# Optimization experiments

Hardware: AMD Instinct MI355X
Metric: run time of the kernel (lower is better)

The kernel has to match this reference:

```python
import jax, jax.numpy as jnp
import numpy as np

DIM = 384
DIM_HEAD = 384
HEADS = 4
SCALE = (DIM_HEAD / HEADS) ** -0.5  # per-head dim 96


def _chan_layernorm(x, g, eps=1e-5):
    # LayerNorm over channel dim (axis=1), biased variance, scale only
    mean = jnp.mean(x, axis=1, keepdims=True)
    var = jnp.var(x, axis=1, keepdims=True)
    return (x - mean) * jax.lax.rsqrt(var + eps) * g


def setup_inputs() -> dict:
    key = jax.random.key(0)
    k0, k1, k2 = jax.random.split(key, 3)
    x = jax.random.normal(k0, (16, DIM, 64, 64), dtype=jnp.float32)
    prenorm_g = jnp.ones((1, DIM, 1, 1), dtype=jnp.float32)
    Wqkv = jax.random.normal(k1, (3 * DIM_HEAD, DIM), dtype=jnp.float32) * 0.02
    Wout = jax.random.normal(k2, (DIM, DIM_HEAD), dtype=jnp.float32) * 0.02
    bout = jnp.zeros((DIM,), dtype=jnp.float32)
    outnorm_g = jnp.ones((1, DIM, 1, 1), dtype=jnp.float32)
    return {"x": x, "prenorm_g": prenorm_g, "Wqkv": Wqkv,
            "Wout": Wout, "bout": bout, "outnorm_g": outnorm_g}


def reference(x, prenorm_g, Wqkv, Wout, bout, outnorm_g):
    b, c, h, w = x.shape
    n = h * w
    ch = DIM_HEAD // HEADS  # per-head channels

    xn = _chan_layernorm(x, prenorm_g)              # prenorm; residual uses this
    qkv = jnp.einsum('oc,bchw->bohw', Wqkv, xn)     # 1x1 conv, no bias
    q, k, v = jnp.split(qkv, 3, axis=1)             # each [b, dim_head, h, w]

    def to_heads(t):
        return t.reshape(b, HEADS, ch, n)           # b h c (x y)
    q, k, v = to_heads(q), to_heads(k), to_heads(v)

    q = jax.nn.softmax(q, axis=2) * SCALE           # softmax over channel dim
    k = jax.nn.softmax(k, axis=3)                   # softmax over spatial dim

    context = jnp.einsum('bhdn,bhen->bhde', k, v)   # [b,h,ch,ch]
    out = jnp.einsum('bhde,bhdn->bhen', context, q) # [b,h,ch,n]
    out = out.reshape(b, DIM_HEAD, h, w)

    out = jnp.einsum('oc,bchw->bohw', Wout, out) + bout[None, :, None, None]
    out = _chan_layernorm(out, outnorm_g)
    return out + xn
```

## Files before the change

kernel.cpp:

```cpp
#include <hip/hip_runtime.h>
#include <cstdint>
#include <cstddef>


#define P_     65536
#define P96_   6291456
#define ROW_   384
#define NS_    8
#define CHK_   512
#define SCALE_ 0.10206207261596577f
#define EPS_   1e-5f

typedef unsigned short us16;
typedef __attribute__((ext_vector_type(8))) unsigned short ushort8;
typedef __attribute__((ext_vector_type(8))) short short8;
typedef __attribute__((ext_vector_type(4))) float f32x4;
typedef __attribute__((ext_vector_type(2))) unsigned int uint2v;

static __device__ __forceinline__ float bfu2f(us16 u) {
  union { float f; unsigned int i; } x; x.i = ((unsigned int)u) << 16; return x.f;
}
static __device__ __forceinline__ us16 f2bfu(float f) {
  union { float f; unsigned int u; } x; x.f = f;
  unsigned int r = x.u + 0x7fffu + ((x.u >> 16) & 1u);
  return (us16)(r >> 16);
}

#define GLDS16(gp, lp) \
  __builtin_amdgcn_global_load_lds((const __attribute__((address_space(1))) void*)(gp), \
                                   (__attribute__((address_space(3))) void*)(lp), 16, 0, 0)

__global__ __launch_bounds__(256) void k_wcvt(const float* __restrict__ wqkv,
                                              const float* __restrict__ wout,
                                              us16* __restrict__ wbf) {
  int i = (blockIdx.x * 256 + threadIdx.x) * 4;
  const float* s = (i < 442368) ? (wqkv + i) : (wout + (i - 442368));
  wbf[i + 0] = f2bfu(s[0]); wbf[i + 1] = f2bfu(s[1]);
  wbf[i + 2] = f2bfu(s[2]); wbf[i + 3] = f2bfu(s[3]);
}

__global__ __launch_bounds__(256) void k_prenorm(const float* __restrict__ x,
                                                 const float* __restrict__ g,
                                                 us16* __restrict__ xn) {
  __shared__ float gs[384];
  __shared__ float sm[4][64], sq[4][64];
  int t = threadIdx.x;
  for (int c = t; c < 384; c += 256) gs[c] = g[c];
  int qd = t >> 6, pb = t & 63;
  int p = blockIdx.x * 64 + pb;
  int b = p >> 12, pix = p & 4095;
  const float* xb = x + (size_t)b * 1572864 + pix;
  float xv[96];
  float s1 = 0.f, s2 = 0.f;
  #pragma unroll
  for (int i = 0; i < 96; ++i) {
    float v = xb[(size_t)(qd * 96 + i) * 4096];
    xv[i] = v; s1 += v; s2 += v * v;
  }
  sm[qd][pb] = s1; sq[qd][pb] = s2;
  __syncthreads();
  float su = sm[0][pb] + sm[1][pb] + sm[2][pb] + sm[3][pb];
  float ss = sq[0][pb] + sq[1][pb] + sq[2][pb] + sq[3][pb];
  float mean = su * (1.f / 384);
  float var = ss * (1.f / 384) - mean * mean;
  float rs = rsqrtf(var + EPS_);
  us16* ob = xn + (size_t)p * ROW_ + qd * 96;
  #pragma unroll
  for (int c8 = 0; c8 < 12; ++c8) {
    ushort8 u;
    #pragma unroll
    for (int j = 0; j < 8; ++j)
      u[j] = f2bfu((xv[c8 * 8 + j] - mean) * rs * gs[qd * 96 + c8 * 8 + j]);
    *(ushort8*)(ob + c8 * 8) = u;
  }
}

__global__ __launch_bounds__(512, 2) void k_gemm(const us16* __restrict__ src,
                                                 const us16* __restrict__ W,
                                                 us16* __restrict__ dst,
                                                 int MT, int mode) {
  __shared__ __align__(16) us16 As[3 * 16384];
  __shared__ __align__(16) us16 Bs[3 * 8192];
  int i = blockIdx.x;
  int xcd = i & 7, idx = i >> 3;
  int ot = idx % MT;
  int pt = (idx / MT) * 8 + xcd;
  int p0 = pt * 256, o0 = ot * 128;
  int tid = threadIdx.x;
  int wv = tid >> 6, l = tid & 63;
  int wr = wv >> 1, wc = wv & 1;
  int lm = l & 15, kq = l >> 4;
  int lr = l >> 3, lg = l & 7;

  bool rm = (mode != 0) || (ot < 3);
  bool isk = (mode == 0) && (ot >= 3) && (ot < 6);

  const us16* aB[4]; const us16* bB[2];
  int swz = (lg ^ lr) * 8;
  #pragma unroll
  for (int r = 0; r < 4; ++r)
    aB[r] = src + (size_t)(p0 + 64 * r + 8 * wv + lr) * ROW_ + swz;
  #pragma unroll
  for (int r = 0; r < 2; ++r)
    bB[r] = W + (size_t)(o0 + 64 * r + 8 * wv + lr) * ROW_ + swz;

  int aidx[4][2], bidx[4][2];
  #pragma unroll
  for (int ii = 0; ii < 4; ++ii) {
    int row = wr * 64 + ii * 16 + lm;
    #pragma unroll
    for (int ks = 0; ks < 2; ++ks)
      aidx[ii][ks] = row * 8 + ((ks * 4 + kq) ^ (row & 7));
  }
  #pragma unroll
  for (int jj = 0; jj < 4; ++jj) {
    int row = wc * 64 + jj * 16 + lm;
    #pragma unroll
    for (int ks = 0; ks < 2; ++ks)
      bidx[jj][ks] = row * 8 + ((ks * 4 + kq) ^ (row & 7));
  }

  f32x4 acc[4][4];
  #pragma unroll
  for (int a = 0; a < 4; ++a)
    #pragma unroll
    for (int q = 0; q < 4; ++q) acc[a][q] = (f32x4)0.f;

#define STG(t_, b_) do { \
    _Pragma("unroll") \
    for (int r_ = 0; r_ < 4; ++r_) \
      GLDS16(aB[r_] + (t_) * 64, &As[(b_) * 16384 + (64 * r_ + 8 * wv) * 64]); \
    _Pragma("unroll") \
    for (int r_ = 0; r_ < 2; ++r_) \
      GLDS16(bB[r_] + (t_) * 64, &Bs[(b_) * 8192 + (64 * r_ + 8 * wv) * 64]); \
  } while (0)

  STG(0, 0);
  STG(1, 1);
  asm volatile("s_waitcnt vmcnt(6)\n\ts_barrier" ::: "memory");

  #pragma unroll
  for (int t = 0; t < 6; ++t) {
    if (t + 2 < 6) STG(t + 2, (t + 2) % 3);
    const short8* A8 = (const short8*)As + (t % 3) * 2048;
    const short8* B8 = (const short8*)Bs + (t % 3) * 1024;
    __builtin_amdgcn_s_setprio(1);
    #pragma unroll
    for (int ks = 0; ks < 2; ++ks) {
      short8 af[4], bf[4];
      #pragma unroll
      for (int ii = 0; ii < 4; ++ii) af[ii] = A8[aidx[ii][ks]];
      #pragma unroll
      for (int jj = 0; jj < 4; ++jj) bf[jj] = B8[bidx[jj][ks]];
      if (rm) {
        #pragma unroll
        for (int ii = 0; ii < 4; ++ii)
          #pragma unroll
          for (int jj = 0; jj < 4; ++jj)
            acc[ii][jj] = __builtin_amdgcn_mfma_f32_16x16x32_bf16(bf[jj], af[ii], acc[ii][jj], 0, 0, 0);
      } else {
        #pragma unroll
        for (int ii = 0; ii < 4; ++ii)
          #pragma unroll
          for (int jj = 0; jj < 4; ++jj)
            acc[ii][jj] = __builtin_amdgcn_mfma_f32_16x16x32_bf16(af[ii], bf[jj], acc[ii][jj], 0, 0, 0);
      }
    }
    __builtin_amdgcn_s_setprio(0);
    if (t < 5) {
      if (t + 2 < 6)
        asm volatile("s_waitcnt vmcnt(6) lgkmcnt(0)\n\ts_barrier" ::: "memory");
      else
        asm volatile("s_waitcnt vmcnt(0) lgkmcnt(0)\n\ts_barrier" ::: "memory");
    }
  }
#undef STG

  __syncthreads();
  us16* Cs = As;
  const int MS = rm ? 136 : 264;
  #pragma unroll
  for (int ii = 0; ii < 4; ++ii) {
    #pragma unroll
    for (int jj = 0; jj < 4; ++jj) {
      f32x4 v = acc[ii][jj];
      if (isk) {
        #pragma unroll
        for (int r = 0; r < 4; ++r) v[r] = __expf(v[r]);
      }
      alignas(8) us16 b4[4];
      #pragma unroll
      for (int r = 0; r < 4; ++r) b4[r] = f2bfu(v[r]);
      int maj = rm ? (wr * 64 + ii * 16 + lm) : (wc * 64 + jj * 16 + lm);
      int mnr = rm ? (wc * 64 + jj * 16 + kq * 4) : (wr * 64 + ii * 16 + kq * 4);
      *(uint2v*)&Cs[maj * MS + mnr] = *(const uint2v*)b4;
    }
  }
  __syncthreads();

  if (!rm) {
    #pragma unroll
    for (int it = 0; it < 8; ++it) {
      int c = it * 512 + tid;
      int o_l = c >> 5, p8 = c & 31;
      int o = o0 + o_l, sec = o / 96, d = o - sec * 96;
      ushort8 u = *(const ushort8*)&Cs[o_l * 264 + p8 * 8];
      *(ushort8*)(dst + (size_t)sec * P96_ + (size_t)d * P_ + p0 + p8 * 8) = u;
    }
  } else if (mode) {
    #pragma unroll
    for (int it = 0; it < 8; ++it) {
      int c = it * 512 + tid;
      int p_l = c >> 4, ch = c & 15;
      ushort8 u = *(const ushort8*)&Cs[p_l * 136 + ch * 8];
      *(ushort8*)(dst + (size_t)(p0 + p_l) * ROW_ + o0 + ch * 8) = u;
    }
  } else {
    #pragma unroll
    for (int it = 0; it < 8; ++it) {
      int c = it * 512 + tid;
      int p_l = c >> 4, ch = c & 15;
      int o = o0 + ch * 8, sec = o / 96, d = o - sec * 96;
      ushort8 u = *(const ushort8*)&Cs[p_l * 136 + ch * 8];
      *(ushort8*)(dst + (size_t)sec * P96_ + (size_t)(p0 + p_l) * 96 + d) = u;
    }
  }
}

__global__ __launch_bounds__(256) void k_ctx(const us16* __restrict__ qkv,
                                             float* __restrict__ ctxs,
                                             float* __restrict__ zs) {
  __shared__ __align__(16) us16 Ek[96 * 64];
  __shared__ __align__(16) us16 Vv[96 * 64];
  int bh = blockIdx.x, s = blockIdx.y;
  int b = bh >> 2, h = bh & 3;
  const us16* kb = qkv + (size_t)(4 + h) * P96_;
  const us16* vb = qkv + (size_t)(8 + h) * P96_;
  int pbase = b * 4096 + s * CHK_;
  int t = threadIdx.x;
  int wv = t >> 6, l = t & 63;
  int wr = wv >> 1, wc = wv & 1;
  int lm = l & 15, kq = l >> 4;

  f32x4 acc[3][3];
  f32x4 accz[3];
  #pragma unroll
  for (int a = 0; a < 3; ++a) {
    accz[a] = (f32x4)0.f;
    #pragma unroll
    for (int q = 0; q < 3; ++q) acc[a][q] = (f32x4)0.f;
  }
  short8 vone;
  #pragma unroll
  for (int j = 0; j < 8; ++j) vone[j] = (short)0x3F80;

  int srow = wv * 24 + (l >> 3);
  int sgrp = l & 7;

  for (int tile = 0; tile < CHK_ / 64; ++tile) {
    int p0 = pbase + tile * 64;
    #pragma unroll
    for (int c = 0; c < 3; ++c) {
      int r = srow + c * 8;
      int g = sgrp ^ (r & 7);
      GLDS16(kb + (size_t)r * P_ + p0 + g * 8, &Ek[(wv * 24 + c * 8) * 64]);
      GLDS16(vb + (size_t)r * P_ + p0 + g * 8, &Vv[(wv * 24 + c * 8) * 64]);
    }
    __syncthreads();
    const short8* A8 = (const short8*)Ek;
    const short8* B8 = (const short8*)Vv;
    #pragma unroll
    for (int ks = 0; ks < 2; ++ks) {
      short8 af[3], bf[3];
      #pragma unroll
      for (int ii = 0; ii < 3; ++ii) {
        int m = wr * 48 + ii * 16 + lm;
        af[ii] = A8[m * 8 + (((ks * 4 + kq) ^ m) & 7) + ((ks * 4 + kq) & 8)];
        int e = wc * 48 + ii * 16 + lm;
        bf[ii] = B8[e * 8 + (((ks * 4 + kq) ^ e) & 7) + ((ks * 4 + kq) & 8)];
      }
      #pragma unroll
      for (int ii = 0; ii < 3; ++ii)
        #pragma unroll
        for (int jj = 0; jj < 3; ++jj)
          acc[ii][jj] = __builtin_amdgcn_mfma_f32_16x16x32_bf16(af[ii], bf[jj], acc[ii][jj], 0, 0, 0);
      if (wc == 0) {
        #pragma unroll
        for (int ii = 0; ii < 3; ++ii)
          accz[ii] = __builtin_amdgcn_mfma_f32_16x16x32_bf16(af[ii], vone, accz[ii], 0, 0, 0);
      }
    }
    __syncthreads();
  }

  float* cb = ctxs + (size_t)(s * 64 + bh) * 9216;
  #pragma unroll
  for (int ii = 0; ii < 3; ++ii) {
    int m0 = wr * 48 + ii * 16 + kq * 4;
    #pragma unroll
    for (int jj = 0; jj < 3; ++jj) {
      int e = wc * 48 + jj * 16 + lm;
      #pragma unroll
      for (int r = 0; r < 4; ++r)
        cb[(size_t)(m0 + r) * 96 + e] = acc[ii][jj][r];
    }
  }
  if (wc == 0 && lm == 0) {
    #pragma unroll
    for (int ii = 0; ii < 3; ++ii) {
      int m0 = wr * 48 + ii * 16 + kq * 4;
      #pragma unroll
      for (int r = 0; r < 4; ++r)
        zs[(size_t)(s * 64 + bh) * 96 + m0 + r] = accz[ii][r];
    }
  }
}

__global__ __launch_bounds__(256) void k_ctxred(const float* __restrict__ ctxs,
                                                const float* __restrict__ zs,
                                                float* __restrict__ ctx,
                                                float* __restrict__ zr) {
  int bh = blockIdx.x / 9, part = blockIdx.x % 9;
  int t = threadIdx.x;
  int idx = part * 1024 + t * 4;
  f32x4 sum = (f32x4)0.f;
  #pragma unroll
  for (int s = 0; s < NS_; ++s)
    sum += *(const f32x4*)&ctxs[(size_t)(s * 64 + bh) * 9216 + idx];
  *(f32x4*)&ctx[(size_t)bh * 9216 + idx] = sum;
  if (part == 0 && t < 96) {
    float z = 0.f;
    #pragma unroll
    for (int s = 0; s < NS_; ++s) z += zs[(size_t)(s * 64 + bh) * 96 + t];
    zr[bh * 96 + t] = z;
  }
}

__global__ __launch_bounds__(256) void k_attout(const us16* __restrict__ qkv,
                                                const float* __restrict__ ctx,
                                                const float* __restrict__ zr,
                                                us16* __restrict__ attout) {
  __shared__ float cs[9216];
  __shared__ float zrs[96];
  int bh = blockIdx.y, b = bh >> 2, h = bh & 3;
  int t = threadIdx.x;
  const float* cb = ctx + (size_t)bh * 9216;
  for (int i = t; i < 9216; i += 256) cs[i] = cb[i];
  if (t < 96) zrs[t] = 1.0f / zr[bh * 96 + t];
  __syncthreads();
  int p = b * 4096 + blockIdx.x * 256 + t;
  const us16* qrow = qkv + (size_t)h * P96_ + (size_t)p * 96;
  float qv[96];
  #pragma unroll
  for (int c8 = 0; c8 < 12; ++c8) {
    ushort8 u = *(const ushort8*)(qrow + c8 * 8);
    #pragma unroll
    for (int j = 0; j < 8; ++j) qv[c8 * 8 + j] = bfu2f(u[j]);
  }
  float m = -1e30f;
  #pragma unroll
  for (int d = 0; d < 96; ++d) m = fmaxf(m, qv[d]);
  float s = 0.f;
  #pragma unroll
  for (int d = 0; d < 96; ++d) { qv[d] = __expf(qv[d] - m); s += qv[d]; }
  float sc = SCALE_ / s;
  #pragma unroll
  for (int d = 0; d < 96; ++d) qv[d] *= sc * zrs[d];
  us16* ob = attout + (size_t)p * ROW_ + h * 96;
  #pragma unroll 1
  for (int e0 = 0; e0 < 96; e0 += 8) {
    float a0 = 0, a1 = 0, a2 = 0, a3 = 0, a4 = 0, a5 = 0, a6 = 0, a7 = 0;
    #pragma unroll
    for (int d = 0; d < 96; ++d) {
      float qd = qv[d];
      f32x4 c0 = *(const f32x4*)&cs[d * 96 + e0];
      f32x4 c1 = *(const f32x4*)&cs[d * 96 + e0 + 4];
      a0 += qd * c0[0]; a1 += qd * c0[1]; a2 += qd * c0[2]; a3 += qd * c0[3];
      a4 += qd * c1[0]; a5 += qd * c1[1]; a6 += qd * c1[2]; a7 += qd * c1[3];
    }
    ushort8 u;
    u[0] = f2bfu(a0); u[1] = f2bfu(a1); u[2] = f2bfu(a2); u[3] = f2bfu(a3);
    u[4] = f2bfu(a4); u[5] = f2bfu(a5); u[6] = f2bfu(a6); u[7] = f2bfu(a7);
    *(ushort8*)(ob + e0) = u;
  }
}

__global__ __launch_bounds__(256) void k_outnorm(const us16* __restrict__ y,
                                                 const us16* __restrict__ xn,
                                                 const float* __restrict__ bout,
                                                 const float* __restrict__ g,
                                                 float* __restrict__ out) {
  __shared__ float bs[384], gs[384];
  int t = threadIdx.x;
  for (int c = t; c < 384; c += 256) { bs[c] = bout[c]; gs[c] = g[c]; }
  __syncthreads();
  int p = blockIdx.x * 256 + t;
  int b = p >> 12, pix = p & 4095;
  const us16* yb = y + (size_t)p * ROW_;
  const us16* xb = xn + (size_t)p * ROW_;
  float sum = 0.f, sq = 0.f;
  #pragma unroll 4
  for (int c8 = 0; c8 < 48; ++c8) {
    ushort8 u = *(const ushort8*)(yb + c8 * 8);
    #pragma unroll
    for (int j = 0; j < 8; ++j) {
      float v = bfu2f(u[j]) + bs[c8 * 8 + j];
      sum += v; sq += v * v;
    }
  }
  float mean = sum * (1.f / 384);
  float var = sq * (1.f / 384) - mean * mean;
  float rs = rsqrtf(var + EPS_);
  float* oB = out + (size_t)b * 1572864 + pix;
  #pragma unroll 2
  for (int c8 = 0; c8 < 48; ++c8) {
    ushort8 u = *(const ushort8*)(yb + c8 * 8);
    ushort8 ux = *(const ushort8*)(xb + c8 * 8);
    #pragma unroll
    for (int j = 0; j < 8; ++j) {
      int c = c8 * 8 + j;
      float v = bfu2f(u[j]) + bs[c];
      oB[(size_t)c * 4096] = (v - mean) * rs * gs[c] + bfu2f(ux[j]);
    }
  }
}

extern "C" void kernel_launch(void* const* d_in, const int* in_sizes, int n_in,
                              void* d_out, int out_size, void* d_ws, size_t ws_size,
                              hipStream_t stream) {
  const float* x    = (const float*)d_in[0];
  const float* pg   = (const float*)d_in[1];
  const float* wqkv = (const float*)d_in[2];
  const float* wout = (const float*)d_in[3];
  const float* bout = (const float*)d_in[4];
  const float* og   = (const float*)d_in[5];

  char* ws = (char*)d_ws;
  us16*  xn     = (us16*)(ws);
  us16*  qkv    = (us16*)(ws + 50331648);
  us16*  attout = (us16*)(ws + 201326592);
  float* ctxred = (float*)(ws + 251658240);
  float* zred   = (float*)(ws + 254017536);
  us16*  wbf    = (us16*)(ws + 254042112);
  us16*  y      = qkv;
  float* out    = (float*)d_out;
  float* ctxs = (float*)d_out;
  float* zs   = (float*)((char*)d_out + 18874368);

  k_wcvt<<<576, 256, 0, stream>>>(wqkv, wout, wbf);
  k_prenorm<<<1024, 256, 0, stream>>>(x, pg, xn);
  k_gemm<<<2304, 512, 0, stream>>>(xn, wbf, qkv, 9, 0);
  k_ctx<<<dim3(64, NS_), 256, 0, stream>>>(qkv, ctxs, zs);
  k_ctxred<<<576, 256, 0, stream>>>(ctxs, zs, ctxred, zred);
  k_attout<<<dim3(16, 64), 256, 0, stream>>>(qkv, ctxred, zred, attout);
  k_gemm<<<768, 512, 0, stream>>>(attout, wbf + 442368, y, 3, 1);
  k_outnorm<<<256, 256, 0, stream>>>(y, xn, bout, og, out);
}
```

Measured before the change: 476.8 us.

## Fold per-batch context into output projection weights, replacing scalar attout kernel

Instead of computing context^T·q per pixel with scalar FMAs and then applying Wout, the change precomputes a per-batch matrix M = Wout·(context/z)^T with MFMA (context split into bf16 hi/lo parts for precision). The softmaxed, scaled q is written directly, and the final GEMM uses the per-batch M as its weights. This removes the expensive scalar per-pixel 96x96 contraction and the attout intermediate. In exchange it adds a small per-batch weight GEMM and bf16 rounding of the fused matrix.

Result: faster. 434.7 us (-8.8%).

```diff
diff --git a/kernel.cpp b/kernel.cpp
--- a/kernel.cpp
+++ b/kernel.cpp
@@ -94,6 +94,7 @@
 
   bool rm = (mode != 0) || (ot < 3);
   bool isk = (mode == 0) && (ot >= 3) && (ot < 6);
+  const us16* Wb = (mode != 0) ? (W + (size_t)(p0 >> 12) * 147456) : W;
 
   const us16* aB[4]; const us16* bB[2];
   int swz = (lg ^ lr) * 8;
@@ -102,7 +103,7 @@
     aB[r] = src + (size_t)(p0 + 64 * r + 8 * wv + lr) * ROW_ + swz;
   #pragma unroll
   for (int r = 0; r < 2; ++r)
-    bB[r] = W + (size_t)(o0 + 64 * r + 8 * wv + lr) * ROW_ + swz;
+    bB[r] = Wb + (size_t)(o0 + 64 * r + 8 * wv + lr) * ROW_ + swz;
 
   int aidx[4][2], bidx[4][2];
   #pragma unroll
@@ -336,52 +337,115 @@
   }
 }
 
-__global__ __launch_bounds__(256) void k_attout(const us16* __restrict__ qkv,
-                                                const float* __restrict__ ctx,
-                                                const float* __restrict__ zr,
-                                                us16* __restrict__ attout) {
-  __shared__ float cs[9216];
-  __shared__ float zrs[96];
-  int bh = blockIdx.y, b = bh >> 2, h = bh & 3;
+__global__ __launch_bounds__(256) void k_ctxw(const float* __restrict__ ctx,
+                                              const float* __restrict__ zr,
+                                              const us16* __restrict__ wout,
+                                              us16* __restrict__ Mt) {
+  __shared__ __align__(16) us16 Aw[192 * 104];
+  __shared__ __align__(16) us16 Bh[96 * 104];
+  __shared__ __align__(16) us16 Bl[96 * 104];
+  int bh = blockIdx.x >> 1, half = blockIdx.x & 1;
+  int b = bh >> 2, h = bh & 3;
+  int o0 = half * 192;
   int t = threadIdx.x;
+
+  #pragma unroll
+  for (int it = 0; it < 9; ++it) {
+    int c = it * 256 + t;
+    int row = c / 12, e8 = c % 12;
+    ushort8 u = *(const ushort8*)(wout + (size_t)(o0 + row) * 384 + h * 96 + e8 * 8);
+    *(ushort8*)&Aw[row * 104 + e8 * 8] = u;
+  }
   const float* cb = ctx + (size_t)bh * 9216;
-  for (int i = t; i < 9216; i += 256) cs[i] = cb[i];
-  if (t < 96) zrs[t] = 1.0f / zr[bh * 96 + t];
+  #pragma unroll
+  for (int it = 0; it < 9; ++it) {
+    int c = it * 256 + t;
+    int fi = c * 4;
+    int row = fi / 96, e = fi % 96;
+    f32x4 v = *(const f32x4*)&cb[fi];
+    alignas(8) us16 hi[4], lo[4];
+    #pragma unroll
+    for (int r = 0; r < 4; ++r) {
+      hi[r] = f2bfu(v[r]);
+      lo[r] = f2bfu(v[r] - bfu2f(hi[r]));
+    }
+    *(uint2v*)&Bh[row * 104 + e] = *(const uint2v*)hi;
+    *(uint2v*)&Bl[row * 104 + e] = *(const uint2v*)lo;
+  }
   __syncthreads();
-  int p = b * 4096 + blockIdx.x * 256 + t;
-  const us16* qrow = qkv + (size_t)h * P96_ + (size_t)p * 96;
-  float qv[96];
-  #pragma unroll
-  for (int c8 = 0; c8 < 12; ++c8) {
-    ushort8 u = *(const ushort8*)(qrow + c8 * 8);
-    #pragma unroll
-    for (int j = 0; j < 8; ++j) qv[c8 * 8 + j] = bfu2f(u[j]);
-  }
-  float m = -1e30f;
-  #pragma unroll
-  for (int d = 0; d < 96; ++d) m = fmaxf(m, qv[d]);
-  float s = 0.f;
-  #pragma unroll
-  for (int d = 0; d < 96; ++d) { qv[d] = __expf(qv[d] - m); s += qv[d]; }
-  float sc = SCALE_ / s;
-  #pragma unroll
-  for (int d = 0; d < 96; ++d) qv[d] *= sc * zrs[d];
-  us16* ob = attout + (size_t)p * ROW_ + h * 96;
+
+  int wv = t >> 6, l = t & 63;
+  int lm = l & 15, kq = l >> 4;
+  f32x4 acc[3][6];
+  #pragma unroll
+  for (int a = 0; a < 3; ++a)
+    #pragma unroll
+    for (int q = 0; q < 6; ++q) acc[a][q] = (f32x4)0.f;
+
+  const short8* A8 = (const short8*)Aw;
+  const short8* B8h = (const short8*)Bh;
+  const short8* B8l = (const short8*)Bl;
+  #pragma unroll
+  for (int ks = 0; ks < 3; ++ks) {
+    short8 af[3];
+    #pragma unroll
+    for (int ii = 0; ii < 3; ++ii)
+      af[ii] = A8[(wv * 48 + ii * 16 + lm) * 13 + ks * 4 + kq];
+    #pragma unroll
+    for (int jj = 0; jj < 6; ++jj) {
+      short8 bh8 = B8h[(jj * 16 + lm) * 13 + ks * 4 + kq];
+      short8 bl8 = B8l[(jj * 16 + lm) * 13 + ks * 4 + kq];
+      #pragma unroll
+      for (int ii = 0; ii < 3; ++ii) {
+        acc[ii][jj] = __builtin_amdgcn_mfma_f32_16x16x32_bf16(af[ii], bh8, acc[ii][jj], 0, 0, 0);
+        acc[ii][jj] = __builtin_amdgcn_mfma_f32_16x16x32_bf16(af[ii], bl8, acc[ii][jj], 0, 0, 0);
+      }
+    }
+  }
+
+  us16* mb = Mt + (size_t)b * 147456;
+  #pragma unroll
+  for (int jj = 0; jj < 6; ++jj) {
+    int d = jj * 16 + lm;
+    float zinv = 1.0f / zr[bh * 96 + d];
+    #pragma unroll
+    for (int ii = 0; ii < 3; ++ii) {
+      int orow = o0 + wv * 48 + ii * 16 + kq * 4;
+      #pragma unroll
+      for (int r = 0; r < 4; ++r)
+        mb[(size_t)(orow + r) * 384 + h * 96 + d] = f2bfu(acc[ii][jj][r] * zinv);
+    }
+  }
+}
+
+__global__ __launch_bounds__(256) void k_qsm(const us16* __restrict__ qkv,
+                                             us16* __restrict__ Qp) {
+  int p = blockIdx.x * 256 + threadIdx.x;
   #pragma unroll 1
-  for (int e0 = 0; e0 < 96; e0 += 8) {
-    float a0 = 0, a1 = 0, a2 = 0, a3 = 0, a4 = 0, a5 = 0, a6 = 0, a7 = 0;
-    #pragma unroll
-    for (int d = 0; d < 96; ++d) {
-      float qd = qv[d];
-      f32x4 c0 = *(const f32x4*)&cs[d * 96 + e0];
-      f32x4 c1 = *(const f32x4*)&cs[d * 96 + e0 + 4];
-      a0 += qd * c0[0]; a1 += qd * c0[1]; a2 += qd * c0[2]; a3 += qd * c0[3];
-      a4 += qd * c1[0]; a5 += qd * c1[1]; a6 += qd * c1[2]; a7 += qd * c1[3];
-    }
-    ushort8 u;
-    u[0] = f2bfu(a0); u[1] = f2bfu(a1); u[2] = f2bfu(a2); u[3] = f2bfu(a3);
-    u[4] = f2bfu(a4); u[5] = f2bfu(a5); u[6] = f2bfu(a6); u[7] = f2bfu(a7);
-    *(ushort8*)(ob + e0) = u;
+  for (int h = 0; h < 4; ++h) {
+    const us16* qrow = qkv + (size_t)h * P96_ + (size_t)p * 96;
+    float qv[96];
+    #pragma unroll
+    for (int c8 = 0; c8 < 12; ++c8) {
+      ushort8 u = *(const ushort8*)(qrow + c8 * 8);
+      #pragma unroll
+      for (int j = 0; j < 8; ++j) qv[c8 * 8 + j] = bfu2f(u[j]);
+    }
+    float m = -1e30f;
+    #pragma unroll
+    for (int d = 0; d < 96; ++d) m = fmaxf(m, qv[d]);
+    float s = 0.f;
+    #pragma unroll
+    for (int d = 0; d < 96; ++d) { qv[d] = __expf(qv[d] - m); s += qv[d]; }
+    float sc = SCALE_ / s;
+    us16* ob = Qp + (size_t)p * ROW_ + h * 96;
+    #pragma unroll
+    for (int c8 = 0; c8 < 12; ++c8) {
+      ushort8 u;
+      #pragma unroll
+      for (int j = 0; j < 8; ++j) u[j] = f2bfu(qv[c8 * 8 + j] * sc);
+      *(ushort8*)(ob + c8 * 8) = u;
+    }
   }
 }
 
@@ -438,7 +502,7 @@
   char* ws = (char*)d_ws;
   us16*  xn     = (us16*)(ws);
   us16*  qkv    = (us16*)(ws + 50331648);
-  us16*  attout = (us16*)(ws + 201326592);
+  us16*  Qp     = (us16*)(ws + 201326592);
   float* ctxred = (float*)(ws + 251658240);
   float* zred   = (float*)(ws + 254017536);
   us16*  wbf    = (us16*)(ws + 254042112);
@@ -446,13 +510,15 @@
   float* out    = (float*)d_out;
   float* ctxs = (float*)d_out;
   float* zs   = (float*)((char*)d_out + 18874368);
+  us16*  Mt   = (us16*)((char*)d_out + 19070976);
 
   k_wcvt<<<576, 256, 0, stream>>>(wqkv, wout, wbf);
   k_prenorm<<<1024, 256, 0, stream>>>(x, pg, xn);
   k_gemm<<<2304, 512, 0, stream>>>(xn, wbf, qkv, 9, 0);
   k_ctx<<<dim3(64, NS_), 256, 0, stream>>>(qkv, ctxs, zs);
   k_ctxred<<<576, 256, 0, stream>>>(ctxs, zs, ctxred, zred);
-  k_attout<<<dim3(16, 64), 256, 0, stream>>>(qkv, ctxred, zred, attout);
-  k_gemm<<<768, 512, 0, stream>>>(attout, wbf + 442368, y, 3, 1);
+  k_ctxw<<<128, 256, 0, stream>>>(ctxred, zred, wbf + 442368, Mt);
+  k_qsm<<<256, 256, 0, stream>>>(qkv, Qp);
+  k_gemm<<<768, 512, 0, stream>>>(Qp, Mt, y, 3, 1);
   k_outnorm<<<256, 256, 0, stream>>>(y, xn, bout, og, out);
 }
```
